# Optimization experiments

Measured on AMD Instinct MI355X. Metric: run time of the kernel, lower is better.

## Reference

```python
import jax, jax.numpy as jnp
import numpy as np
from jax import lax

INSZ, HSZ, NLAYERS = 1024, 1024, 2
B, T = 32, 512
FORGET_BIAS = 1.0


def setup_inputs() -> dict:
    key = jax.random.key(0)
    ks = jax.random.split(key, 6)
    x = jax.random.normal(ks[0], (B, T, INSZ), dtype=jnp.float32)
    lengths = jax.random.randint(ks[1], (B,), 1, T + 1, dtype=jnp.int32)
    s0 = 1.0 / np.sqrt(INSZ + HSZ)
    s1 = 1.0 / np.sqrt(HSZ + HSZ)
    W0 = jax.random.uniform(ks[2], (INSZ + HSZ, 4 * HSZ), jnp.float32, -s0, s0)
    b0 = jnp.zeros((4 * HSZ,), jnp.float32)
    W1 = jax.random.uniform(ks[3], (HSZ + HSZ, 4 * HSZ), jnp.float32, -s1, s1)
    b1 = jnp.zeros((4 * HSZ,), jnp.float32)
    return {"x": x, "lengths": lengths, "W0": W0, "b0": b0, "W1": W1, "b1": b1}


def _lstm_layer(x, lengths, W, b):
    # x: [B, T, D_in]; TF LSTMCell gate order (i, j, f, o), forget_bias added to f.
    bsz = x.shape[0]
    hsz = b.shape[0] // 4
    tsteps = jnp.arange(x.shape[1])

    def step(carry, inp):
        h, c = carry
        xt, t = inp
        z = jnp.concatenate([xt, h], axis=-1) @ W + b  # [B, 4H]
        i, j, f, o = jnp.split(z, 4, axis=-1)
        c_new = jax.nn.sigmoid(f + FORGET_BIAS) * c + jax.nn.sigmoid(i) * jnp.tanh(j)
        h_new = jax.nn.sigmoid(o) * jnp.tanh(c_new)
        mask = (t < lengths)[:, None]
        # dynamic_rnn: zero outputs past sequence_length, freeze state
        h_out = jnp.where(mask, h_new, 0.0)
        h_keep = jnp.where(mask, h_new, h)
        c_keep = jnp.where(mask, c_new, c)
        return (h_keep, c_keep), h_out

    init = (jnp.zeros((bsz, hsz), x.dtype), jnp.zeros((bsz, hsz), x.dtype))
    (h_fin, c_fin), ys = lax.scan(step, init, (jnp.swapaxes(x, 0, 1), tsteps))
    return jnp.swapaxes(ys, 0, 1), h_fin, c_fin


def reference(x, lengths, W0, b0, W1, b1):
    out0, _, _ = _lstm_layer(x, lengths, W0, b0)
    out1, h1, c1 = _lstm_layer(out0, lengths, W1, b1)
    return out1, (h1, c1)
```

## Files before the change

### kernel.cpp

```cpp
#include <hip/hip_runtime.h>
#include <hip/hip_bf16.h>

typedef unsigned short u16;
typedef unsigned int u32;
typedef unsigned long long u64;
typedef short s8v __attribute__((ext_vector_type(8)));
typedef float f4v __attribute__((ext_vector_type(4)));

#define BQ 32
#define TQ 512
#define DQ 1024
#define CHUNK 128
#define NCHUNK (TQ / CHUNK)
#define NTHR 256
#define NBLK_R 256

__device__ __host__ inline u16 f2bf(float f) {
    union { float f; unsigned u; } v; v.f = f;
    unsigned r = v.u + 0x7fffu + ((v.u >> 16) & 1u);
    return (u16)(r >> 16);
}
__device__ __host__ inline float bf2f(u16 u) {
    union { unsigned u; float f; } v; v.u = ((unsigned)u) << 16;
    return v.f;
}

__global__ void init_kernel(u32* __restrict__ z0, size_t n0,
                            u32* __restrict__ z1, size_t n1) {
    size_t i = (size_t)blockIdx.x * blockDim.x + threadIdx.x;
    size_t stride = (size_t)gridDim.x * blockDim.x;
    for (size_t idx = i; idx < n0; idx += stride) z0[idx] = 0;
    for (size_t idx = i; idx < n1; idx += stride) z1[idx] = 0;
}

__device__ inline void unpack_pk(uint4 A, uint4 B, s8v& hi, s8v& lo) {
    union { u32 u[4]; s8v v; } H, L;
    H.u[0] = (A.x >> 16) | (A.y & 0xffff0000u); L.u[0] = (A.x & 0xffffu) | (A.y << 16);
    H.u[1] = (A.z >> 16) | (A.w & 0xffff0000u); L.u[1] = (A.z & 0xffffu) | (A.w << 16);
    H.u[2] = (B.x >> 16) | (B.y & 0xffff0000u); L.u[2] = (B.x & 0xffffu) | (B.y << 16);
    H.u[3] = (B.z >> 16) | (B.w & 0xffff0000u); L.u[3] = (B.z & 0xffffu) | (B.w << 16);
    hi = H.v; lo = L.v;
}

__global__ __launch_bounds__(NTHR) void xproj_gemm_kernel(
    const float* __restrict__ in_f32,
    const u32* __restrict__ hh,
    const int* __restrict__ lens,
    const float* __restrict__ W,
    const float* __restrict__ bias,
    float* __restrict__ zx,
    int t0)
{
    __shared__ u16 As[2][128][40];
    __shared__ u16 Bs[2][128][40];

    const int tid = threadIdx.x;
    const int bm = blockIdx.x & 31;
    const int bn = blockIdx.x >> 5;

    const int wv = tid >> 6;
    const int wm = wv >> 1, wn = wv & 1;
    const int lane = tid & 63;
    const int frow = lane & 15;
    const int quad = lane >> 4;

    const int am = tid >> 1;
    const int akh = (tid & 1) * 16;
    const int amg = bm * 128 + am;
    const int ab = amg >> 7;
    const int atl = amg & 127;
    const int at = t0 + atl;

    const int bk = tid >> 3;
    const int bng = (tid & 7) * 16;

    bool arow_live = true;
    size_t arow;
    if (in_f32) {
        arow = ((size_t)ab * TQ + at) * DQ;
    } else {
        arow = ((size_t)(at + 1) * BQ + ab) * DQ;
        arow_live = (at < lens[ab]);
    }

    f4v acc[4][4];
    #pragma unroll
    for (int i = 0; i < 4; ++i)
        #pragma unroll
        for (int j = 0; j < 4; ++j) acc[i][j] = (f4v){0.f, 0.f, 0.f, 0.f};

    for (int kt = 0; kt < 32; ++kt) {
        const int k0 = kt * 32;
        if (in_f32) {
            const float* src = in_f32 + arow + k0 + akh;
            #pragma unroll
            for (int j4 = 0; j4 < 4; ++j4) {
                float4 v = ((const float4*)src)[j4];
                float vv[4] = {v.x, v.y, v.z, v.w};
                #pragma unroll
                for (int e = 0; e < 4; ++e) {
                    u16 hh16 = f2bf(vv[e]);
                    As[0][am][akh + j4 * 4 + e] = hh16;
                    As[1][am][akh + j4 * 4 + e] = f2bf(vv[e] - bf2f(hh16));
                }
            }
        } else {
            const u32* src = hh + arow + k0 + akh;
            #pragma unroll
            for (int j4 = 0; j4 < 4; ++j4) {
                uint4 v = ((const uint4*)src)[j4];
                if (!arow_live) { v.x = v.y = v.z = v.w = 0; }
                u32 vv[4] = {v.x, v.y, v.z, v.w};
                #pragma unroll
                for (int e = 0; e < 4; ++e) {
                    As[0][am][akh + j4 * 4 + e] = (u16)(vv[e] >> 16);
                    As[1][am][akh + j4 * 4 + e] = (u16)(vv[e] & 0xffffu);
                }
            }
        }
        {
            const float* wsrc = W + (size_t)(k0 + bk) * (4 * DQ) + bn * 128 + bng;
            #pragma unroll
            for (int j4 = 0; j4 < 4; ++j4) {
                float4 v = ((const float4*)wsrc)[j4];
                float vv[4] = {v.x, v.y, v.z, v.w};
                #pragma unroll
                for (int e = 0; e < 4; ++e) {
                    u16 hh16 = f2bf(vv[e]);
                    int n = bng + j4 * 4 + e;
                    Bs[0][n][bk] = hh16;
                    Bs[1][n][bk] = f2bf(vv[e] - bf2f(hh16));
                }
            }
        }
        __syncthreads();

        s8v ah[4], al[4], bh[4], bl[4];
        #pragma unroll
        for (int mt = 0; mt < 4; ++mt) {
            ah[mt] = *(const s8v*)&As[0][wm * 64 + mt * 16 + frow][quad * 8];
            al[mt] = *(const s8v*)&As[1][wm * 64 + mt * 16 + frow][quad * 8];
        }
        #pragma unroll
        for (int nt = 0; nt < 4; ++nt) {
            bh[nt] = *(const s8v*)&Bs[0][wn * 64 + nt * 16 + frow][quad * 8];
            bl[nt] = *(const s8v*)&Bs[1][wn * 64 + nt * 16 + frow][quad * 8];
        }
        #pragma unroll
        for (int mt = 0; mt < 4; ++mt)
            #pragma unroll
            for (int nt = 0; nt < 4; ++nt) {
                acc[mt][nt] = __builtin_amdgcn_mfma_f32_16x16x32_bf16(ah[mt], bh[nt], acc[mt][nt], 0, 0, 0);
                acc[mt][nt] = __builtin_amdgcn_mfma_f32_16x16x32_bf16(al[mt], bh[nt], acc[mt][nt], 0, 0, 0);
                acc[mt][nt] = __builtin_amdgcn_mfma_f32_16x16x32_bf16(ah[mt], bl[nt], acc[mt][nt], 0, 0, 0);
            }
        __syncthreads();
    }

    float bv[4];
    #pragma unroll
    for (int nt = 0; nt < 4; ++nt) bv[nt] = bias[bn * 128 + wn * 64 + nt * 16 + frow];
    #pragma unroll
    for (int mt = 0; mt < 4; ++mt) {
        #pragma unroll
        for (int nt = 0; nt < 4; ++nt) {
            int col = bn * 128 + wn * 64 + nt * 16 + frow;
            #pragma unroll
            for (int r = 0; r < 4; ++r) {
                int row = bm * 128 + wm * 64 + mt * 16 + quad * 4 + r;
                zx[(size_t)row * (4 * DQ) + col] = acc[mt][nt][r] + bv[nt];
            }
        }
    }
}

__global__ __launch_bounds__(NTHR, 1) void lstm_rec_kernel(
    const float* __restrict__ zx,
    const float* __restrict__ W,
    const int* __restrict__ lens,
    u32* __restrict__ hh,
    u32* __restrict__ subc,
    u32* __restrict__ topc,
    float* __restrict__ state_h,
    float* __restrict__ state_c,
    float* __restrict__ out_f32,
    float* __restrict__ hc_out,
    int t0, int is_last)
{
    __shared__ u16 wt[2][32][1032];
    __shared__ float red[4][16][36];

    const int tid = threadIdx.x;
    const int blk = blockIdx.x;
    const int bg = blk & 1;
    const int cg = blk >> 1;
    const int grp = (blk >> 1) & 7;

    for (int idx = tid; idx < 32 * 1024; idx += NTHR) {
        int n = idx & 31, k = idx >> 5;
        int c = n >> 2, g = n & 3;
        float w = W[(size_t)(DQ + k) * (4 * DQ) + g * DQ + cg * 8 + c];
        u16 wh = f2bf(w);
        wt[0][n][k] = wh;
        wt[1][n][k] = f2bf(w - bf2f(wh));
    }

    const int gb_l = tid >> 3;
    const int gc = tid & 7;
    const int b_g = bg * 16 + gb_l;
    const int hcol = cg * 8 + gc;
    float c_state = 0.f, h_state = 0.f;
    int mylen = 0;
    if (tid < 128) {
        mylen = lens[b_g];
        h_state = state_h[(size_t)b_g * DQ + hcol];
        c_state = state_c[(size_t)b_g * DQ + hcol];
    }

    const int wave = tid >> 6;
    const int lane = tid & 63;
    const int frow = lane & 15;
    const int quad = lane >> 4;
    const int ksrc = wave * 256;

    __syncthreads();

    const int tend = t0 + CHUNK;
    for (int t = t0; t < tend; ++t) {
        const u32* hp = hh + ((size_t)t * BQ + (bg * 16 + frow)) * DQ + ksrc + quad * 8;
        uint4 q[16];
        #pragma unroll
        for (int s = 0; s < 8; ++s) {
            q[2 * s]     = ((const uint4*)(hp + s * 32))[0];
            q[2 * s + 1] = ((const uint4*)(hp + s * 32))[1];
        }

        f4v acc0 = {0.f, 0.f, 0.f, 0.f};
        f4v acc1 = {0.f, 0.f, 0.f, 0.f};
        #pragma unroll
        for (int s = 0; s < 8; ++s) {
            s8v a_h, a_l;
            unpack_pk(q[2 * s], q[2 * s + 1], a_h, a_l);
            const int koff = ksrc + s * 32 + quad * 8;
            s8v b0h = *(const s8v*)&wt[0][frow][koff];
            s8v b0l = *(const s8v*)&wt[1][frow][koff];
            s8v b1h = *(const s8v*)&wt[0][16 + frow][koff];
            s8v b1l = *(const s8v*)&wt[1][16 + frow][koff];
            acc0 = __builtin_amdgcn_mfma_f32_16x16x32_bf16(a_h, b0h, acc0, 0, 0, 0);
            acc1 = __builtin_amdgcn_mfma_f32_16x16x32_bf16(a_h, b1h, acc1, 0, 0, 0);
            acc0 = __builtin_amdgcn_mfma_f32_16x16x32_bf16(a_l, b0h, acc0, 0, 0, 0);
            acc1 = __builtin_amdgcn_mfma_f32_16x16x32_bf16(a_l, b1h, acc1, 0, 0, 0);
            acc0 = __builtin_amdgcn_mfma_f32_16x16x32_bf16(a_h, b0l, acc0, 0, 0, 0);
            acc1 = __builtin_amdgcn_mfma_f32_16x16x32_bf16(a_h, b1l, acc1, 0, 0, 0);
        }
        #pragma unroll
        for (int r = 0; r < 4; ++r) {
            red[wave][quad * 4 + r][frow] = acc0[r];
            red[wave][quad * 4 + r][16 + frow] = acc1[r];
        }

        float zxv[4];
        if (tid < 128) {
            size_t base = ((size_t)b_g * CHUNK + (t - t0)) * (4 * DQ) + hcol;
            #pragma unroll
            for (int g = 0; g < 4; ++g) zxv[g] = zx[base + (size_t)g * DQ];
        }
        __syncthreads();

        if (tid < 128) {
            float z[4];
            #pragma unroll
            for (int g = 0; g < 4; ++g) {
                int n = gc * 4 + g;
                z[g] = red[0][gb_l][n] + red[1][gb_l][n] + red[2][gb_l][n] + red[3][gb_l][n]
                     + zxv[g];
            }
            float si = 1.f / (1.f + __expf(-z[0]));
            float sf = 1.f / (1.f + __expf(-(z[2] + 1.0f)));
            float so = 1.f / (1.f + __expf(-z[3]));
            float cn = sf * c_state + si * tanhf(z[1]);
            float hn = so * tanhf(cn);
            bool m = (t < mylen);
            float hk = m ? hn : h_state;
            float ck = m ? cn : c_state;
            h_state = hk; c_state = ck;

            u16 hh16 = f2bf(hk);
            u16 hl16 = f2bf(hk - bf2f(hh16));
            u32 packed = ((u32)hh16 << 16) | (u32)hl16;
            __hip_atomic_store(hh + ((size_t)(t + 1) * BQ + b_g) * DQ + hcol,
                               packed, __ATOMIC_RELAXED, __HIP_MEMORY_SCOPE_AGENT);

            if (is_last) {
                float ho = m ? hn : 0.f;
                out_f32[((size_t)b_g * TQ + t) * DQ + hcol] = ho;
            }
        }

        asm volatile("s_waitcnt vmcnt(0)" ::: "memory");
        __syncthreads();
        if (t < tend - 1) {
            if (tid == 0) {
                u32* sc = &subc[((t * 2 + bg) * 8 + grp) * 16];
                u32* tc = &topc[(t * 2 + bg) * 16];
                u32 old = atomicAdd(sc, 1u);
                if (old == 15) atomicAdd(tc, 1u);
                while (__hip_atomic_load(tc, __ATOMIC_RELAXED,
                                         __HIP_MEMORY_SCOPE_AGENT) < 8) { }
            }
            __syncthreads();
        }
    }

    if (tid < 128) {
        state_h[(size_t)b_g * DQ + hcol] = h_state;
        state_c[(size_t)b_g * DQ + hcol] = c_state;
        if (is_last && tend == TQ) {
            hc_out[(size_t)b_g * DQ + hcol] = h_state;
            hc_out[(size_t)BQ * DQ + (size_t)b_g * DQ + hcol] = c_state;
        }
    }
}

extern "C" void kernel_launch(void* const* d_in, const int* in_sizes, int n_in,
                              void* d_out, int out_size, void* d_ws, size_t ws_size,
                              hipStream_t stream) {
    const float* x    = (const float*)d_in[0];
    const int*   lens = (const int*)d_in[1];
    const float* W0   = (const float*)d_in[2];
    const float* b0   = (const float*)d_in[3];
    const float* W1   = (const float*)d_in[4];
    const float* b1   = (const float*)d_in[5];
    float* out = (float*)d_out;

    const size_t N   = (size_t)BQ * TQ * DQ;
    const size_t ZXN = (size_t)BQ * CHUNK * 4 * DQ;
    const size_t HD  = (size_t)BQ * DQ;

    float* zx  = (float*)d_ws;
    u32* hh    = (u32*)(zx + ZXN);
    float* sh0 = (float*)(hh + (size_t)(TQ + 1) * HD);
    float* sc0 = sh0 + HD;
    float* sh1 = sc0 + HD;
    float* sc1 = sh1 + HD;
    u32* sub0  = (u32*)(sc1 + HD);
    u32* top0  = sub0 + (size_t)TQ * 2 * 8 * 16;
    u32* sub1  = top0 + (size_t)TQ * 2 * 16;
    u32* top1  = sub1 + (size_t)TQ * 2 * 8 * 16;
    u32* zend  = top1 + (size_t)TQ * 2 * 16;
    const size_t nzero = (size_t)(zend - (u32*)sh0);

    init_kernel<<<256, 256, 0, stream>>>(hh, HD, (u32*)sh0, nzero);

    for (int c = 0; c < NCHUNK; ++c) {
        int t0 = c * CHUNK;
        xproj_gemm_kernel<<<1024, NTHR, 0, stream>>>(x, nullptr, lens, W0, b0, zx, t0);
        lstm_rec_kernel<<<NBLK_R, NTHR, 0, stream>>>(
            zx, W0, lens, hh, sub0, top0, sh0, sc0,
            nullptr, nullptr, t0, 0);
    }
    for (int c = 0; c < NCHUNK; ++c) {
        int t0 = c * CHUNK;
        xproj_gemm_kernel<<<1024, NTHR, 0, stream>>>(nullptr, hh, lens, W1, b1, zx, t0);
        lstm_rec_kernel<<<NBLK_R, NTHR, 0, stream>>>(
            zx, W1, lens, hh, sub1, top1, sh1, sc1,
            out, out + N, t0, 1);
    }
}
```

Measured before the change: 7.433 ms.

## Replace grid-wide step barrier with poison-flag dataflow sync on hidden state

Removes the per-timestep hierarchical atomic counter barrier across recurrent blocks. Each block now fills the hidden-state buffer with a poison value and spins, using cache-bypassing loads, until the h slices it needs are no longer poisoned. Extra kernels re-poison hh before each layer-1 chunk. The change also hoists the zx load ahead of the matmul, double-buffers the reduction scratch, and splits the MFMA accumulators to shorten dependency chains. It relies on a real h value never packing to 0xFFFFFFFF (a NaN pattern), and it adds poison-fill passes over the hh buffer.

```diff
diff --git a/kernel.cpp b/kernel.cpp
--- a/kernel.cpp
+++ b/kernel.cpp
@@ -6,6 +6,7 @@
 typedef unsigned long long u64;
 typedef short s8v __attribute__((ext_vector_type(8)));
 typedef float f4v __attribute__((ext_vector_type(4)));
+typedef u32 u32x4 __attribute__((ext_vector_type(4)));
 
 #define BQ 32
 #define TQ 512
@@ -15,6 +16,8 @@
 #define NTHR 256
 #define NBLK_R 256
 
+#define HPOISON 0xFFFFFFFFu
+
 __device__ __host__ inline u16 f2bf(float f) {
     union { float f; unsigned u; } v; v.f = f;
     unsigned r = v.u + 0x7fffu + ((v.u >> 16) & 1u);
@@ -25,20 +28,27 @@
     return v.f;
 }
 
-__global__ void init_kernel(u32* __restrict__ z0, size_t n0,
-                            u32* __restrict__ z1, size_t n1) {
+__global__ void init_kernel(u32* __restrict__ hh, u32* __restrict__ z1, size_t n1) {
+    const size_t HD = (size_t)BQ * DQ;
     size_t i = (size_t)blockIdx.x * blockDim.x + threadIdx.x;
     size_t stride = (size_t)gridDim.x * blockDim.x;
-    for (size_t idx = i; idx < n0; idx += stride) z0[idx] = 0;
+    for (size_t idx = i; idx < HD; idx += stride) hh[idx] = 0;
+    for (size_t idx = i; idx < (size_t)TQ * HD; idx += stride) hh[HD + idx] = HPOISON;
     for (size_t idx = i; idx < n1; idx += stride) z1[idx] = 0;
 }
 
-__device__ inline void unpack_pk(uint4 A, uint4 B, s8v& hi, s8v& lo) {
+__global__ void poison_kernel(u32* __restrict__ p, size_t n) {
+    size_t i = (size_t)blockIdx.x * blockDim.x + threadIdx.x;
+    size_t stride = (size_t)gridDim.x * blockDim.x;
+    for (size_t idx = i; idx < n; idx += stride) p[idx] = HPOISON;
+}
+
+__device__ inline void unpack_pk(u32x4 A, u32x4 B, s8v& hi, s8v& lo) {
     union { u32 u[4]; s8v v; } H, L;
-    H.u[0] = (A.x >> 16) | (A.y & 0xffff0000u); L.u[0] = (A.x & 0xffffu) | (A.y << 16);
-    H.u[1] = (A.z >> 16) | (A.w & 0xffff0000u); L.u[1] = (A.z & 0xffffu) | (A.w << 16);
-    H.u[2] = (B.x >> 16) | (B.y & 0xffff0000u); L.u[2] = (B.x & 0xffffu) | (B.y << 16);
-    H.u[3] = (B.z >> 16) | (B.w & 0xffff0000u); L.u[3] = (B.z & 0xffffu) | (B.w << 16);
+    H.u[0] = (A[0] >> 16) | (A[1] & 0xffff0000u); L.u[0] = (A[0] & 0xffffu) | (A[1] << 16);
+    H.u[1] = (A[2] >> 16) | (A[3] & 0xffff0000u); L.u[1] = (A[2] & 0xffffu) | (A[3] << 16);
+    H.u[2] = (B[0] >> 16) | (B[1] & 0xffff0000u); L.u[2] = (B[0] & 0xffffu) | (B[1] << 16);
+    H.u[3] = (B[2] >> 16) | (B[3] & 0xffff0000u); L.u[3] = (B[2] & 0xffffu) | (B[3] << 16);
     hi = H.v; lo = L.v;
 }
 
@@ -179,8 +189,6 @@
     const float* __restrict__ W,
     const int* __restrict__ lens,
     u32* __restrict__ hh,
-    u32* __restrict__ subc,
-    u32* __restrict__ topc,
     float* __restrict__ state_h,
     float* __restrict__ state_c,
     float* __restrict__ out_f32,
@@ -188,13 +196,12 @@
     int t0, int is_last)
 {
     __shared__ u16 wt[2][32][1032];
-    __shared__ float red[4][16][36];
+    __shared__ float red[2][4][16][36];
 
     const int tid = threadIdx.x;
     const int blk = blockIdx.x;
     const int bg = blk & 1;
     const int cg = blk >> 1;
-    const int grp = (blk >> 1) & 7;
 
     for (int idx = tid; idx < 32 * 1024; idx += NTHR) {
         int n = idx & 31, k = idx >> 5;
@@ -227,16 +234,51 @@
 
     const int tend = t0 + CHUNK;
     for (int t = t0; t < tend; ++t) {
+        float zxv[4];
+        if (tid < 128) {
+            size_t base = ((size_t)b_g * CHUNK + (t - t0)) * (4 * DQ) + hcol;
+            #pragma unroll
+            for (int g = 0; g < 4; ++g) zxv[g] = zx[base + (size_t)g * DQ];
+        }
+
         const u32* hp = hh + ((size_t)t * BQ + (bg * 16 + frow)) * DQ + ksrc + quad * 8;
-        uint4 q[16];
+        u32x4 q[16];
         #pragma unroll
         for (int s = 0; s < 8; ++s) {
-            q[2 * s]     = ((const uint4*)(hp + s * 32))[0];
-            q[2 * s + 1] = ((const uint4*)(hp + s * 32))[1];
-        }
-
-        f4v acc0 = {0.f, 0.f, 0.f, 0.f};
-        f4v acc1 = {0.f, 0.f, 0.f, 0.f};
+            q[2 * s]     = *(const u32x4*)(hp + s * 32);
+            q[2 * s + 1] = *(const u32x4*)(hp + s * 32 + 4);
+        }
+        u32 bad = 0;
+        #pragma unroll
+        for (int i = 0; i < 16; ++i)
+            if (q[i][0] == HPOISON || q[i][1] == HPOISON ||
+                q[i][2] == HPOISON || q[i][3] == HPOISON)
+                bad |= 1u << i;
+
+        while (__any(bad != 0u)) {
+            if (bad) {
+                #pragma unroll
+                for (int i = 0; i < 16; ++i)
+                    if (bad & (1u << i)) {
+                        const u32* ap = hp + (i >> 1) * 32 + (i & 1) * 4;
+                        asm volatile("global_load_dwordx4 %0, %1, off sc0 sc1"
+                                     : "=&v"(q[i]) : "v"(ap));
+                    }
+            }
+            asm volatile("s_waitcnt vmcnt(0)" ::: "memory");
+            __builtin_amdgcn_sched_barrier(0);
+            u32 nb = 0;
+            #pragma unroll
+            for (int i = 0; i < 16; ++i)
+                if ((bad & (1u << i)) &&
+                    (q[i][0] == HPOISON || q[i][1] == HPOISON ||
+                     q[i][2] == HPOISON || q[i][3] == HPOISON))
+                    nb |= 1u << i;
+            bad = nb;
+        }
+
+        f4v acc0 = {0.f,0.f,0.f,0.f}, acc1 = {0.f,0.f,0.f,0.f};
+        f4v acc2 = {0.f,0.f,0.f,0.f}, acc3 = {0.f,0.f,0.f,0.f};
         #pragma unroll
         for (int s = 0; s < 8; ++s) {
             s8v a_h, a_l;
@@ -246,24 +288,23 @@
             s8v b0l = *(const s8v*)&wt[1][frow][koff];
             s8v b1h = *(const s8v*)&wt[0][16 + frow][koff];
             s8v b1l = *(const s8v*)&wt[1][16 + frow][koff];
-            acc0 = __builtin_amdgcn_mfma_f32_16x16x32_bf16(a_h, b0h, acc0, 0, 0, 0);
-            acc1 = __builtin_amdgcn_mfma_f32_16x16x32_bf16(a_h, b1h, acc1, 0, 0, 0);
-            acc0 = __builtin_amdgcn_mfma_f32_16x16x32_bf16(a_l, b0h, acc0, 0, 0, 0);
-            acc1 = __builtin_amdgcn_mfma_f32_16x16x32_bf16(a_l, b1h, acc1, 0, 0, 0);
-            acc0 = __builtin_amdgcn_mfma_f32_16x16x32_bf16(a_h, b0l, acc0, 0, 0, 0);
-            acc1 = __builtin_amdgcn_mfma_f32_16x16x32_bf16(a_h, b1l, acc1, 0, 0, 0);
-        }
+            f4v& A0 = (s & 1) ? acc2 : acc0;
+            f4v& A1 = (s & 1) ? acc3 : acc1;
+            A0 = __builtin_amdgcn_mfma_f32_16x16x32_bf16(a_h, b0h, A0, 0, 0, 0);
+            A1 = __builtin_amdgcn_mfma_f32_16x16x32_bf16(a_h, b1h, A1, 0, 0, 0);
+            A0 = __builtin_amdgcn_mfma_f32_16x16x32_bf16(a_l, b0h, A0, 0, 0, 0);
+            A1 = __builtin_amdgcn_mfma_f32_16x16x32_bf16(a_l, b1h, A1, 0, 0, 0);
+            A0 = __builtin_amdgcn_mfma_f32_16x16x32_bf16(a_h, b0l, A0, 0, 0, 0);
+            A1 = __builtin_amdgcn_mfma_f32_16x16x32_bf16(a_h, b1l, A1, 0, 0, 0);
+        }
+        acc0 += acc2;
+        acc1 += acc3;
+
+        const int pb = t & 1;
         #pragma unroll
         for (int r = 0; r < 4; ++r) {
-            red[wave][quad * 4 + r][frow] = acc0[r];
-            red[wave][quad * 4 + r][16 + frow] = acc1[r];
-        }
-
-        float zxv[4];
-        if (tid < 128) {
-            size_t base = ((size_t)b_g * CHUNK + (t - t0)) * (4 * DQ) + hcol;
-            #pragma unroll
-            for (int g = 0; g < 4; ++g) zxv[g] = zx[base + (size_t)g * DQ];
+            red[pb][wave][quad * 4 + r][frow] = acc0[r];
+            red[pb][wave][quad * 4 + r][16 + frow] = acc1[r];
         }
         __syncthreads();
 
@@ -272,8 +313,8 @@
             #pragma unroll
             for (int g = 0; g < 4; ++g) {
                 int n = gc * 4 + g;
-                z[g] = red[0][gb_l][n] + red[1][gb_l][n] + red[2][gb_l][n] + red[3][gb_l][n]
-                     + zxv[g];
+                z[g] = red[pb][0][gb_l][n] + red[pb][1][gb_l][n]
+                     + red[pb][2][gb_l][n] + red[pb][3][gb_l][n] + zxv[g];
             }
             float si = 1.f / (1.f + __expf(-z[0]));
             float sf = 1.f / (1.f + __expf(-(z[2] + 1.0f)));
@@ -295,20 +336,6 @@
                 float ho = m ? hn : 0.f;
                 out_f32[((size_t)b_g * TQ + t) * DQ + hcol] = ho;
             }
-        }
-
-        asm volatile("s_waitcnt vmcnt(0)" ::: "memory");
-        __syncthreads();
-        if (t < tend - 1) {
-            if (tid == 0) {
-                u32* sc = &subc[((t * 2 + bg) * 8 + grp) * 16];
-                u32* tc = &topc[(t * 2 + bg) * 16];
-                u32 old = atomicAdd(sc, 1u);
-                if (old == 15) atomicAdd(tc, 1u);
-                while (__hip_atomic_load(tc, __ATOMIC_RELAXED,
-                                         __HIP_MEMORY_SCOPE_AGENT) < 8) { }
-            }
-            __syncthreads();
         }
     }
 
@@ -343,27 +370,22 @@
     float* sc0 = sh0 + HD;
     float* sh1 = sc0 + HD;
     float* sc1 = sh1 + HD;
-    u32* sub0  = (u32*)(sc1 + HD);
-    u32* top0  = sub0 + (size_t)TQ * 2 * 8 * 16;
-    u32* sub1  = top0 + (size_t)TQ * 2 * 16;
-    u32* top1  = sub1 + (size_t)TQ * 2 * 8 * 16;
-    u32* zend  = top1 + (size_t)TQ * 2 * 16;
-    const size_t nzero = (size_t)(zend - (u32*)sh0);
-
-    init_kernel<<<256, 256, 0, stream>>>(hh, HD, (u32*)sh0, nzero);
+    const size_t nzero = 4 * HD;
+
+    init_kernel<<<1024, 256, 0, stream>>>(hh, (u32*)sh0, nzero);
 
     for (int c = 0; c < NCHUNK; ++c) {
         int t0 = c * CHUNK;
         xproj_gemm_kernel<<<1024, NTHR, 0, stream>>>(x, nullptr, lens, W0, b0, zx, t0);
         lstm_rec_kernel<<<NBLK_R, NTHR, 0, stream>>>(
-            zx, W0, lens, hh, sub0, top0, sh0, sc0,
-            nullptr, nullptr, t0, 0);
+            zx, W0, lens, hh, sh0, sc0, nullptr, nullptr, t0, 0);
     }
     for (int c = 0; c < NCHUNK; ++c) {
         int t0 = c * CHUNK;
         xproj_gemm_kernel<<<1024, NTHR, 0, stream>>>(nullptr, hh, lens, W1, b1, zx, t0);
+        poison_kernel<<<256, 256, 0, stream>>>(hh + (size_t)(t0 + 1) * HD,
+                                               (size_t)CHUNK * HD);
         lstm_rec_kernel<<<NBLK_R, NTHR, 0, stream>>>(
-            zx, W1, lens, hh, sub1, top1, sh1, sc1,
-            out, out + N, t0, 1);
-    }
-}
+            zx, W1, lens, hh, sh1, sc1, out, out + N, t0, 1);
+    }
+}
```

Result: slower. 9.770 ms (+31.4%).

## Pre-pack weights and inputs into transposed hi/lo bf16 pairs before GEMM

Applied to the files above, without the earlier changes.

Adds kernels that convert W (transposed to N-major) and each x chunk into packed u32 hi/lo bf16 split pairs once, so the x-projection GEMM only does vector copies into shared memory. The GEMM then unpacks the pairs from LDS with unpack_pk instead of doing per-element float-to-bf16 conversion and scattered transposed LDS stores for W in every tile. This removes redundant conversion work repeated across the 32 M-blocks and the strided B loads. In exchange it adds extra kernel launches, extra workspace, and a full read/write pass over W and x.

```diff
diff --git a/kernel.cpp b/kernel.cpp
--- a/kernel.cpp
+++ b/kernel.cpp
@@ -24,6 +24,11 @@
     union { unsigned u; float f; } v; v.u = ((unsigned)u) << 16;
     return v.f;
 }
+__device__ inline u32 packsplit(float f) {
+    u16 hi = f2bf(f);
+    u16 lo = f2bf(f - bf2f(hi));
+    return ((u32)hi << 16) | (u32)lo;
+}
 
 __global__ void init_kernel(u32* __restrict__ z0, size_t n0,
                             u32* __restrict__ z1, size_t n1) {
@@ -31,6 +36,29 @@
     size_t stride = (size_t)gridDim.x * blockDim.x;
     for (size_t idx = i; idx < n0; idx += stride) z0[idx] = 0;
     for (size_t idx = i; idx < n1; idx += stride) z1[idx] = 0;
+}
+
+__global__ void pack_w_kernel(const float* __restrict__ W, u32* __restrict__ wpkT) {
+    size_t i = (size_t)blockIdx.x * blockDim.x + threadIdx.x;
+    size_t stride = (size_t)gridDim.x * blockDim.x;
+    const size_t NTOT = (size_t)4 * DQ * DQ;
+    for (size_t idx = i; idx < NTOT; idx += stride) {
+        size_t n = idx >> 10, k = idx & 1023;
+        wpkT[idx] = packsplit(W[k * (4 * DQ) + n]);
+    }
+}
+
+__global__ void pack_x_kernel(const float* __restrict__ x, u32* __restrict__ xpk,
+                              int t0) {
+    size_t i = (size_t)blockIdx.x * blockDim.x + threadIdx.x;
+    size_t stride = (size_t)gridDim.x * blockDim.x;
+    const size_t NTOT = (size_t)BQ * CHUNK * DQ;
+    for (size_t idx = i; idx < NTOT; idx += stride) {
+        size_t b = idx >> 17;
+        size_t r = idx & 131071;
+        size_t tl = r >> 10, k = r & 1023;
+        xpk[idx] = packsplit(x[((size_t)b * TQ + t0 + tl) * DQ + k]);
+    }
 }
 
 __device__ inline void unpack_pk(uint4 A, uint4 B, s8v& hi, s8v& lo) {
@@ -43,16 +71,15 @@
 }
 
 __global__ __launch_bounds__(NTHR) void xproj_gemm_kernel(
-    const float* __restrict__ in_f32,
-    const u32* __restrict__ hh,
+    const u32* __restrict__ apk,
     const int* __restrict__ lens,
-    const float* __restrict__ W,
+    const u32* __restrict__ wpkT,
     const float* __restrict__ bias,
     float* __restrict__ zx,
-    int t0)
+    int t0, int is_l1)
 {
-    __shared__ u16 As[2][128][40];
-    __shared__ u16 Bs[2][128][40];
+    __shared__ u32 Asp[128][36];
+    __shared__ u32 Bsp[128][36];
 
     const int tid = threadIdx.x;
     const int bm = blockIdx.x & 31;
@@ -71,17 +98,15 @@
     const int atl = amg & 127;
     const int at = t0 + atl;
 
-    const int bk = tid >> 3;
-    const int bng = (tid & 7) * 16;
-
     bool arow_live = true;
     size_t arow;
-    if (in_f32) {
-        arow = ((size_t)ab * TQ + at) * DQ;
+    if (!is_l1) {
+        arow = (size_t)amg * DQ;
     } else {
         arow = ((size_t)(at + 1) * BQ + ab) * DQ;
         arow_live = (at < lens[ab]);
     }
+    const u32* bbase = wpkT + (size_t)(bn * 128 + am) * DQ;
 
     f4v acc[4][4];
     #pragma unroll
@@ -91,46 +116,21 @@
 
     for (int kt = 0; kt < 32; ++kt) {
         const int k0 = kt * 32;
-        if (in_f32) {
-            const float* src = in_f32 + arow + k0 + akh;
-            #pragma unroll
-            for (int j4 = 0; j4 < 4; ++j4) {
-                float4 v = ((const float4*)src)[j4];
-                float vv[4] = {v.x, v.y, v.z, v.w};
-                #pragma unroll
-                for (int e = 0; e < 4; ++e) {
-                    u16 hh16 = f2bf(vv[e]);
-                    As[0][am][akh + j4 * 4 + e] = hh16;
-                    As[1][am][akh + j4 * 4 + e] = f2bf(vv[e] - bf2f(hh16));
-                }
-            }
-        } else {
-            const u32* src = hh + arow + k0 + akh;
+        {
+            const u32* src = apk + arow + k0 + akh;
             #pragma unroll
             for (int j4 = 0; j4 < 4; ++j4) {
                 uint4 v = ((const uint4*)src)[j4];
                 if (!arow_live) { v.x = v.y = v.z = v.w = 0; }
-                u32 vv[4] = {v.x, v.y, v.z, v.w};
-                #pragma unroll
-                for (int e = 0; e < 4; ++e) {
-                    As[0][am][akh + j4 * 4 + e] = (u16)(vv[e] >> 16);
-                    As[1][am][akh + j4 * 4 + e] = (u16)(vv[e] & 0xffffu);
-                }
+                *(uint4*)&Asp[am][akh + 4 * j4] = v;
             }
         }
         {
-            const float* wsrc = W + (size_t)(k0 + bk) * (4 * DQ) + bn * 128 + bng;
+            const u32* src = bbase + k0 + akh;
             #pragma unroll
             for (int j4 = 0; j4 < 4; ++j4) {
-                float4 v = ((const float4*)wsrc)[j4];
-                float vv[4] = {v.x, v.y, v.z, v.w};
-                #pragma unroll
-                for (int e = 0; e < 4; ++e) {
-                    u16 hh16 = f2bf(vv[e]);
-                    int n = bng + j4 * 4 + e;
-                    Bs[0][n][bk] = hh16;
-                    Bs[1][n][bk] = f2bf(vv[e] - bf2f(hh16));
-                }
+                uint4 v = ((const uint4*)src)[j4];
+                *(uint4*)&Bsp[am][akh + 4 * j4] = v;
             }
         }
         __syncthreads();
@@ -138,13 +138,15 @@
         s8v ah[4], al[4], bh[4], bl[4];
         #pragma unroll
         for (int mt = 0; mt < 4; ++mt) {
-            ah[mt] = *(const s8v*)&As[0][wm * 64 + mt * 16 + frow][quad * 8];
-            al[mt] = *(const s8v*)&As[1][wm * 64 + mt * 16 + frow][quad * 8];
+            uint4 a0 = *(const uint4*)&Asp[wm * 64 + mt * 16 + frow][quad * 8];
+            uint4 a1 = *(const uint4*)&Asp[wm * 64 + mt * 16 + frow][quad * 8 + 4];
+            unpack_pk(a0, a1, ah[mt], al[mt]);
         }
         #pragma unroll
         for (int nt = 0; nt < 4; ++nt) {
-            bh[nt] = *(const s8v*)&Bs[0][wn * 64 + nt * 16 + frow][quad * 8];
-            bl[nt] = *(const s8v*)&Bs[1][wn * 64 + nt * 16 + frow][quad * 8];
+            uint4 b0 = *(const uint4*)&Bsp[wn * 64 + nt * 16 + frow][quad * 8];
+            uint4 b1 = *(const uint4*)&Bsp[wn * 64 + nt * 16 + frow][quad * 8 + 4];
+            unpack_pk(b0, b1, bh[nt], bl[nt]);
         }
         #pragma unroll
         for (int mt = 0; mt < 4; ++mt)
@@ -336,6 +338,8 @@
     const size_t N   = (size_t)BQ * TQ * DQ;
     const size_t ZXN = (size_t)BQ * CHUNK * 4 * DQ;
     const size_t HD  = (size_t)BQ * DQ;
+    const size_t WPK = (size_t)4 * DQ * DQ;
+    const size_t XPK = (size_t)BQ * CHUNK * DQ;
 
     float* zx  = (float*)d_ws;
     u32* hh    = (u32*)(zx + ZXN);
@@ -349,19 +353,25 @@
     u32* top1  = sub1 + (size_t)TQ * 2 * 8 * 16;
     u32* zend  = top1 + (size_t)TQ * 2 * 16;
     const size_t nzero = (size_t)(zend - (u32*)sh0);
+    u32* wpk0  = zend;
+    u32* wpk1  = wpk0 + WPK;
+    u32* xpk   = wpk1 + WPK;
 
     init_kernel<<<256, 256, 0, stream>>>(hh, HD, (u32*)sh0, nzero);
+    pack_w_kernel<<<2048, 256, 0, stream>>>(W0, wpk0);
+    pack_w_kernel<<<2048, 256, 0, stream>>>(W1, wpk1);
 
     for (int c = 0; c < NCHUNK; ++c) {
         int t0 = c * CHUNK;
-        xproj_gemm_kernel<<<1024, NTHR, 0, stream>>>(x, nullptr, lens, W0, b0, zx, t0);
+        pack_x_kernel<<<2048, 256, 0, stream>>>(x, xpk, t0);
+        xproj_gemm_kernel<<<1024, NTHR, 0, stream>>>(xpk, lens, wpk0, b0, zx, t0, 0);
         lstm_rec_kernel<<<NBLK_R, NTHR, 0, stream>>>(
             zx, W0, lens, hh, sub0, top0, sh0, sc0,
             nullptr, nullptr, t0, 0);
     }
     for (int c = 0; c < NCHUNK; ++c) {
         int t0 = c * CHUNK;
-        xproj_gemm_kernel<<<1024, NTHR, 0, stream>>>(nullptr, hh, lens, W1, b1, zx, t0);
+        xproj_gemm_kernel<<<1024, NTHR, 0, stream>>>(hh, lens, wpk1, b1, zx, t0, 1);
         lstm_rec_kernel<<<NBLK_R, NTHR, 0, stream>>>(
             zx, W1, lens, hh, sub1, top1, sh1, sc1,
             out, out + N, t0, 1);
```

New measurement: 6.965 ms. -6.3%, faster.
